# Kernel optimization log

Hardware: AMD Instinct MI355X
Metric: run time of the kernel (lower is better)

Reference implementation:

```python
import jax, jax.numpy as jnp
import numpy as np

NUM_NODES = 100_000
NUM_EDGES = 1_200_000
NUM_REL = 3
EMBED_DIM = 64
HIDDEN_DIM = 64
NUM_CLS = 2
NUM_GRAPHS = 512


def setup_inputs() -> dict:
    key = jax.random.key(0)
    ks = jax.random.split(key, 12)
    s = 1.0 / np.sqrt(EMBED_DIM)
    inp = {
        # forward args
        "x": jnp.zeros((NUM_NODES,), dtype=jnp.int64),  # vocab size 1 -> all zeros
        "edge_index": jax.random.randint(ks[0], (2, NUM_EDGES), 0, NUM_NODES, dtype=jnp.int64),
        "edge_type": jax.random.randint(ks[1], (NUM_EDGES,), 0, NUM_REL, dtype=jnp.int64),
        "batch": jnp.sort(jax.random.randint(ks[2], (NUM_NODES,), 0, NUM_GRAPHS, dtype=jnp.int64)),
        # parameters
        "embed_w": jax.random.normal(ks[3], (1, EMBED_DIM), jnp.float32),
        "W1": jax.random.normal(ks[4], (NUM_REL, EMBED_DIM, HIDDEN_DIM), jnp.float32) * s,
        "root1": jax.random.normal(ks[5], (EMBED_DIM, HIDDEN_DIM), jnp.float32) * s,
        "b1": jnp.zeros((HIDDEN_DIM,), jnp.float32),
        "W2": jax.random.normal(ks[6], (NUM_REL, HIDDEN_DIM, HIDDEN_DIM), jnp.float32) * s,
        "root2": jax.random.normal(ks[7], (HIDDEN_DIM, HIDDEN_DIM), jnp.float32) * s,
        "b2": jnp.zeros((HIDDEN_DIM,), jnp.float32),
        "lin_w": jax.random.normal(ks[8], (HIDDEN_DIM, NUM_CLS), jnp.float32) * s,
        "lin_b": jnp.zeros((NUM_CLS,), jnp.float32),
    }
    return inp


def rgcn_conv(h, W, root, b, src, dst, edge_type):
    """PyG RGCNConv with mean aggregation per relation + root weight + bias."""
    n = h.shape[0]
    out = h @ root + b  # root/self contribution, [N, H]
    for r in range(NUM_REL):
        m = (edge_type == r).astype(h.dtype)  # [E]
        tr = h @ W[r]                          # [N, H] small GEMM
        msg = tr[src] * m[:, None]             # gather [E, H]
        ssum = jax.ops.segment_sum(msg, dst, num_segments=n)  # scatter-add [N, H]
        cnt = jax.ops.segment_sum(m, dst, num_segments=n)     # per-relation in-degree
        out = out + ssum / jnp.clip(cnt, 1.0)[:, None]        # mean aggregation
    return out


def reference(x, edge_index, edge_type, batch, embed_w, W1, root1, b1, W2, root2, b2, lin_w, lin_b):
    src, dst = edge_index[0], edge_index[1]
    h = embed_w[x]                                       # [N, D] embedding lookup
    h = jax.nn.relu(rgcn_conv(h, W1, root1, b1, src, dst, edge_type))
    h = jax.nn.relu(rgcn_conv(h, W2, root2, b2, src, dst, edge_type))
    # global mean pool over graphs
    gsum = jax.ops.segment_sum(h, batch, num_segments=NUM_GRAPHS)            # [G, H]
    gcnt = jax.ops.segment_sum(jnp.ones_like(h[:, 0]), batch, num_segments=NUM_GRAPHS)
    g_emb = gsum / jnp.clip(gcnt, 1.0)[:, None]
    return g_emb @ lin_w + lin_b                          # [G, num_cls]
```

## Files before the change

### kernel.cpp

```cpp
#include <hip/hip_runtime.h>

#define NODES   100000
#define EDGES   1200000
#define NREL    3
#define DIM     64
#define NGRAPH  512

#define BSH     8
#define NB      391
#define BUCKCAP 4096
#define NCH     224
#define CHUNK   5360
#define POISON  0xAAAAAAAAu

#define OFF_PSUM  0
#define OFF_PCNT  4096
#define OFF_DONE  6144
#define OFF_ZEND  6400
#define OFF_CUR   6400
#define OFF_MBN   8448
#define OFF_REC   408832
#define OFF_BASE  6814976
#define OFF_T2    6817024

__global__ __launch_bounds__(512) void k_scat_tab(
        const int* __restrict__ ei, const int* __restrict__ et,
        const float* __restrict__ embed_w, const float* __restrict__ W1,
        const float* __restrict__ root1, const float* __restrict__ b1,
        const float* __restrict__ W2, const float* __restrict__ root2,
        const float* __restrict__ b2,
        unsigned int* __restrict__ cursor, unsigned int* __restrict__ rec,
        unsigned char* __restrict__ mbn,
        float* __restrict__ base, float* __restrict__ T2,
        char* __restrict__ ws) {
    const int tid = threadIdx.x;
    const int bid = blockIdx.x;
    if (bid < 32) {
        {
            uint4* z = (uint4*)ws;
            const int gt = bid * 512 + tid;
            if (gt < OFF_ZEND / 16) z[gt] = make_uint4(0, 0, 0, 0);
        }
        __shared__ float h0[DIM];
        __shared__ float u[DIM];
        __shared__ float t[NREL][DIM];
        __shared__ float h1s[8][DIM];
        __shared__ float red[4][DIM];
        const bool act = tid < 256;
        const int j = tid & 63, w = (tid >> 6) & 3;
        if (act && tid < DIM) h0[tid] = embed_w[tid];
        __syncthreads();
        if (act) {
            const float* M = (w == 0) ? root1 : (W1 + (size_t)(w - 1) * DIM * DIM);
            float s = 0.f;
            for (int k = 0; k < DIM; ++k) s += h0[k] * M[k * DIM + j];
            if (w == 0) u[j] = s + b1[j];
            else        t[w - 1][j] = s;
        }
        __syncthreads();
        if (act) {
            for (int p = w; p < 8; p += 4) {
                float v = u[j];
                if (p & 1) v += t[0][j];
                if (p & 2) v += t[1][j];
                if (p & 4) v += t[2][j];
                h1s[p][j] = fmaxf(v, 0.f);
            }
        }
        __syncthreads();
        const int row = bid;
        const int p = (row < 8) ? row : ((row - 8) & 7);
        if (act) {
            const float* M = (row < 8) ? root2
                                       : (W2 + (size_t)((row - 8) >> 3) * DIM * DIM);
            float s = 0.f;
            for (int k = w * 16; k < w * 16 + 16; ++k) s += h1s[p][k] * M[k * DIM + j];
            red[w][j] = s;
        }
        __syncthreads();
        if (act && w == 0) {
            const float v = red[0][j] + red[1][j] + red[2][j] + red[3][j];
            if (row < 8) base[p * DIM + j] = v + b2[j];
            else         T2[(row - 8) * DIM + j] = v;
        }
        return;
    }
    __shared__ unsigned int   srec[CHUNK];
    __shared__ unsigned short sbkt[CHUNK];
    __shared__ int hist[NB];
    __shared__ int cur[NB];
    for (int b = tid; b < NB; b += 512) hist[b] = 0;
    __syncthreads();
    const int e0 = (bid - 32) * CHUNK;
    const int* src = ei;
    const int* dst = ei + EDGES;
    for (int i = tid; i < CHUNK / 4; i += 512) {
        const int e = e0 + i * 4;
        if (e < EDGES) {
            const int4 s4 = *(const int4*)(src + e);
            const int4 d4 = *(const int4*)(dst + e);
            const int4 r4 = *(const int4*)(et + e);
            const int j = i * 4;
            srec[j + 0] = ((unsigned)(d4.x & 255) << 19) | ((unsigned)r4.x << 17) | (unsigned)s4.x;
            sbkt[j + 0] = (unsigned short)(d4.x >> BSH);
            atomicAdd(&hist[d4.x >> BSH], 1);
            mbn[d4.x * 4 + r4.x] = 1;
            srec[j + 1] = ((unsigned)(d4.y & 255) << 19) | ((unsigned)r4.y << 17) | (unsigned)s4.y;
            sbkt[j + 1] = (unsigned short)(d4.y >> BSH);
            atomicAdd(&hist[d4.y >> BSH], 1);
            mbn[d4.y * 4 + r4.y] = 1;
            srec[j + 2] = ((unsigned)(d4.z & 255) << 19) | ((unsigned)r4.z << 17) | (unsigned)s4.z;
            sbkt[j + 2] = (unsigned short)(d4.z >> BSH);
            atomicAdd(&hist[d4.z >> BSH], 1);
            mbn[d4.z * 4 + r4.z] = 1;
            srec[j + 3] = ((unsigned)(d4.w & 255) << 19) | ((unsigned)r4.w << 17) | (unsigned)s4.w;
            sbkt[j + 3] = (unsigned short)(d4.w >> BSH);
            atomicAdd(&hist[d4.w >> BSH], 1);
            mbn[d4.w * 4 + r4.w] = 1;
        }
    }
    __syncthreads();
    for (int b = tid; b < NB; b += 512) {
        const int h = hist[b];
        unsigned off = 0;
        if (h) off = atomicAdd(&cursor[b], (unsigned)h) - POISON;
        cur[b] = b * BUCKCAP + (int)off;
    }
    __syncthreads();
    int nl = EDGES - e0;
    if (nl > CHUNK) nl = CHUNK;
    for (int i = tid; i < nl; i += 512) {
        const int b = sbkt[i];
        const int p = atomicAdd(&cur[b], 1);
        if (p < (b + 1) * BUCKCAP) rec[p] = srec[i];
    }
}

__global__ __launch_bounds__(1024) void k_node(
        const unsigned int* __restrict__ rec, const unsigned int* __restrict__ cursor,
        const unsigned char* __restrict__ mbn, const int* __restrict__ batch,
        const float* __restrict__ base, const float* __restrict__ T2,
        const float* __restrict__ lin_w, const float* __restrict__ lin_b,
        float* __restrict__ psum, int* __restrict__ pcnt,
        int* __restrict__ done, float* __restrict__ out) {
    __shared__ unsigned int h[3072];
    __shared__ float bs[8 * DIM];
    __shared__ float ts[24 * DIM];
    __shared__ int lastflag;
    const int tid = threadIdx.x;
    const unsigned* mbn32 = (const unsigned*)mbn;
    for (int i = tid; i < 3072; i += 1024) h[i] = 0;
    if (tid < 8 * DIM) bs[tid] = base[tid];
    for (int i = tid; i < 24 * DIM; i += 1024) ts[i] = T2[i];
    __syncthreads();
    const int b = blockIdx.x;
    const int s = b * BUCKCAP;
    unsigned un = cursor[b] - POISON;
    int n = (un > BUCKCAP) ? BUCKCAP : (int)un;
    for (int i = tid; i < n; i += 1024) {
        const unsigned r32 = rec[s + i];
        const unsigned x = mbn32[r32 & 0x1FFFF];
        const int p = (x & 1) | ((x >> 7) & 2) | ((x >> 14) & 4);
        const int idx = (r32 >> 19) * 24 + ((r32 >> 17) & 3) * 8 + p;
        atomicAdd(&h[idx >> 1], 1u << ((idx & 1) * 16));
    }
    __syncthreads();
    const int lane = tid & 63;
    const int w = tid >> 6;
    const int v0 = (b << BSH) + w * 16;
    float dummy = 0.f;
    if (v0 < NODES) {
        const float lw0 = lin_w[lane * 2 + 0];
        const float lw1 = lin_w[lane * 2 + 1];
        int pidx = v0 + (lane & 15);
        if (pidx >= NODES) pidx = NODES - 1;
        const int bv = batch[pidx];
        const int mv = (int)mbn32[pidx];
        float acc = 0.f;
        int curg = -1, runlen = 0;
        for (int i = 0; i < 16; ++i) {
            const int v = v0 + i;
            if (v >= NODES) break;
            const int mx = __shfl(mv, i);
            const int pm = (mx & 1) | ((mx >> 7) & 2) | ((mx >> 14) & 4);
            float sacc = bs[pm * DIM + lane];
            const unsigned* hv = &h[(v & 255) * 12];
            #pragma unroll
            for (int r = 0; r < NREL; ++r) {
                const unsigned x0 = hv[r * 4 + 0], x1 = hv[r * 4 + 1];
                const unsigned x2 = hv[r * 4 + 2], x3 = hv[r * 4 + 3];
                const int cr = (int)((x0 & 0xFFFF) + (x0 >> 16) + (x1 & 0xFFFF) + (x1 >> 16)
                                   + (x2 & 0xFFFF) + (x2 >> 16) + (x3 & 0xFFFF) + (x3 >> 16));
                if (cr > 0) {
                    float msg = 0.f;
                    const float* tr = &ts[r * 8 * DIM + lane];
                    if (x0) msg += (float)(x0 & 0xFFFF) * tr[0 * DIM]
                                 + (float)(x0 >> 16)    * tr[1 * DIM];
                    if (x1) msg += (float)(x1 & 0xFFFF) * tr[2 * DIM]
                                 + (float)(x1 >> 16)    * tr[3 * DIM];
                    if (x2) msg += (float)(x2 & 0xFFFF) * tr[4 * DIM]
                                 + (float)(x2 >> 16)    * tr[5 * DIM];
                    if (x3) msg += (float)(x3 & 0xFFFF) * tr[6 * DIM]
                                 + (float)(x3 >> 16)    * tr[7 * DIM];
                    sacc += msg / (float)cr;
                }
            }
            sacc = fmaxf(sacc, 0.f);
            const int g = __shfl(bv, i);
            if (g != curg) {
                if (curg >= 0) {
                    float p0 = acc * lw0, p1 = acc * lw1;
                    #pragma unroll
                    for (int off = 32; off; off >>= 1) {
                        p0 += __shfl_down(p0, off);
                        p1 += __shfl_down(p1, off);
                    }
                    if (lane == 0) {
                        dummy += atomicAdd(&psum[curg * 2 + 0], p0);
                        dummy += atomicAdd(&psum[curg * 2 + 1], p1);
                        dummy += (float)atomicAdd(&pcnt[curg], runlen);
                    }
                }
                curg = g; acc = 0.f; runlen = 0;
            }
            acc += sacc; runlen++;
        }
        if (curg >= 0) {
            float p0 = acc * lw0, p1 = acc * lw1;
            #pragma unroll
            for (int off = 32; off; off >>= 1) {
                p0 += __shfl_down(p0, off);
                p1 += __shfl_down(p1, off);
            }
            if (lane == 0) {
                dummy += atomicAdd(&psum[curg * 2 + 0], p0);
                dummy += atomicAdd(&psum[curg * 2 + 1], p1);
                dummy += (float)atomicAdd(&pcnt[curg], runlen);
            }
        }
    }
    asm volatile("" :: "v"(dummy));
    __syncthreads();
    if (tid == 0) lastflag = (atomicAdd(done, 1) == NB - 1) ? 1 : 0;
    __syncthreads();
    if (lastflag && tid < NGRAPH) {
        const float q0 = atomicAdd(&psum[tid * 2 + 0], 0.0f);
        const float q1 = atomicAdd(&psum[tid * 2 + 1], 0.0f);
        const int   c  = atomicAdd(&pcnt[tid], 0);
        const float inv = 1.0f / fmaxf((float)c, 1.0f);
        out[tid * 2 + 0] = q0 * inv + lin_b[0];
        out[tid * 2 + 1] = q1 * inv + lin_b[1];
    }
}

extern "C" void kernel_launch(void* const* d_in, const int* in_sizes, int n_in,
                              void* d_out, int out_size, void* d_ws, size_t ws_size,
                              hipStream_t stream) {
    const int*   ei      = (const int*)d_in[1];
    const int*   et      = (const int*)d_in[2];
    const int*   batch   = (const int*)d_in[3];
    const float* embed_w = (const float*)d_in[4];
    const float* W1      = (const float*)d_in[5];
    const float* root1   = (const float*)d_in[6];
    const float* b1      = (const float*)d_in[7];
    const float* W2      = (const float*)d_in[8];
    const float* root2   = (const float*)d_in[9];
    const float* b2      = (const float*)d_in[10];
    const float* lin_w   = (const float*)d_in[11];
    const float* lin_b   = (const float*)d_in[12];
    float* out = (float*)d_out;

    char* ws = (char*)d_ws;
    float*         psum = (float*)(ws + OFF_PSUM);
    int*           pcnt = (int*)(ws + OFF_PCNT);
    int*           done = (int*)(ws + OFF_DONE);
    unsigned int*  cur  = (unsigned int*)(ws + OFF_CUR);
    unsigned char* mbn  = (unsigned char*)(ws + OFF_MBN);
    unsigned int*  rec  = (unsigned int*)(ws + OFF_REC);
    float*         base = (float*)(ws + OFF_BASE);
    float*         T2   = (float*)(ws + OFF_T2);

    k_scat_tab<<<256, 512,  0, stream>>>(ei, et, embed_w, W1, root1, b1, W2, root2,
                                         b2, cur, rec, mbn, base, T2, (char*)d_ws);
    k_node    <<<NB,  1024, 0, stream>>>(rec, cur, mbn, batch, base, T2, lin_w,
                                         lin_b, psum, pcnt, done, out);
}
```

Baseline: 139.4 us.

## Split node buckets into quarter-blocks and unroll scatter loads for memory parallelism

k_node now runs four 512-thread blocks per 256-node bucket. Each block filters the bucket's records by destination quarter and keeps a smaller shared histogram, and each wave prefetches the next node's counters into registers. In k_scat_tab the edge-load and scatter loops are manually unrolled so several int4 loads and atomics are in flight per thread. The aim is more blocks and more memory-level parallelism, at the cost of every record being read four times (once per quarter block) and more atomics on the completion counter.

New measurement: 152.8 us. +9.6%, slower.

```diff
diff --git a/kernel.cpp b/kernel.cpp
--- a/kernel.cpp
+++ b/kernel.cpp
@@ -8,6 +8,7 @@
 
 #define BSH     8
 #define NB      391
+#define NBK2    1564
 #define BUCKCAP 4096
 #define NCH     224
 #define CHUNK   5360
@@ -94,29 +95,60 @@
     const int e0 = (bid - 32) * CHUNK;
     const int* src = ei;
     const int* dst = ei + EDGES;
-    for (int i = tid; i < CHUNK / 4; i += 512) {
-        const int e = e0 + i * 4;
-        if (e < EDGES) {
-            const int4 s4 = *(const int4*)(src + e);
-            const int4 d4 = *(const int4*)(dst + e);
-            const int4 r4 = *(const int4*)(et + e);
-            const int j = i * 4;
-            srec[j + 0] = ((unsigned)(d4.x & 255) << 19) | ((unsigned)r4.x << 17) | (unsigned)s4.x;
-            sbkt[j + 0] = (unsigned short)(d4.x >> BSH);
-            atomicAdd(&hist[d4.x >> BSH], 1);
-            mbn[d4.x * 4 + r4.x] = 1;
-            srec[j + 1] = ((unsigned)(d4.y & 255) << 19) | ((unsigned)r4.y << 17) | (unsigned)s4.y;
-            sbkt[j + 1] = (unsigned short)(d4.y >> BSH);
-            atomicAdd(&hist[d4.y >> BSH], 1);
-            mbn[d4.y * 4 + r4.y] = 1;
-            srec[j + 2] = ((unsigned)(d4.z & 255) << 19) | ((unsigned)r4.z << 17) | (unsigned)s4.z;
-            sbkt[j + 2] = (unsigned short)(d4.z >> BSH);
-            atomicAdd(&hist[d4.z >> BSH], 1);
-            mbn[d4.z * 4 + r4.z] = 1;
-            srec[j + 3] = ((unsigned)(d4.w & 255) << 19) | ((unsigned)r4.w << 17) | (unsigned)s4.w;
-            sbkt[j + 3] = (unsigned short)(d4.w >> BSH);
-            atomicAdd(&hist[d4.w >> BSH], 1);
-            mbn[d4.w * 4 + r4.w] = 1;
+    {
+        const int g0 = tid, g1 = tid + 512, g2 = tid + 1024;
+        const int ea = e0 + g0 * 4, eb = e0 + g1 * 4, ec = e0 + g2 * 4;
+        const bool a0 = (g0 < CHUNK / 4) && (ea < EDGES);
+        const bool a1 = (g1 < CHUNK / 4) && (eb < EDGES);
+        const bool a2 = (g2 < CHUNK / 4) && (ec < EDGES);
+        int4 sa, da, ra, sb, db, rb, sc, dc, rc;
+        if (a0) { sa = *(const int4*)(src + ea); da = *(const int4*)(dst + ea); ra = *(const int4*)(et + ea); }
+        if (a1) { sb = *(const int4*)(src + eb); db = *(const int4*)(dst + eb); rb = *(const int4*)(et + eb); }
+        if (a2) { sc = *(const int4*)(src + ec); dc = *(const int4*)(dst + ec); rc = *(const int4*)(et + ec); }
+        if (a0) {
+            const int j = g0 * 4;
+            srec[j + 0] = ((unsigned)(da.x & 255) << 19) | ((unsigned)ra.x << 17) | (unsigned)sa.x;
+            srec[j + 1] = ((unsigned)(da.y & 255) << 19) | ((unsigned)ra.y << 17) | (unsigned)sa.y;
+            srec[j + 2] = ((unsigned)(da.z & 255) << 19) | ((unsigned)ra.z << 17) | (unsigned)sa.z;
+            srec[j + 3] = ((unsigned)(da.w & 255) << 19) | ((unsigned)ra.w << 17) | (unsigned)sa.w;
+            sbkt[j + 0] = (unsigned short)(da.x >> BSH);
+            sbkt[j + 1] = (unsigned short)(da.y >> BSH);
+            sbkt[j + 2] = (unsigned short)(da.z >> BSH);
+            sbkt[j + 3] = (unsigned short)(da.w >> BSH);
+            atomicAdd(&hist[da.x >> BSH], 1); atomicAdd(&hist[da.y >> BSH], 1);
+            atomicAdd(&hist[da.z >> BSH], 1); atomicAdd(&hist[da.w >> BSH], 1);
+            mbn[da.x * 4 + ra.x] = 1; mbn[da.y * 4 + ra.y] = 1;
+            mbn[da.z * 4 + ra.z] = 1; mbn[da.w * 4 + ra.w] = 1;
+        }
+        if (a1) {
+            const int j = g1 * 4;
+            srec[j + 0] = ((unsigned)(db.x & 255) << 19) | ((unsigned)rb.x << 17) | (unsigned)sb.x;
+            srec[j + 1] = ((unsigned)(db.y & 255) << 19) | ((unsigned)rb.y << 17) | (unsigned)sb.y;
+            srec[j + 2] = ((unsigned)(db.z & 255) << 19) | ((unsigned)rb.z << 17) | (unsigned)sb.z;
+            srec[j + 3] = ((unsigned)(db.w & 255) << 19) | ((unsigned)rb.w << 17) | (unsigned)sb.w;
+            sbkt[j + 0] = (unsigned short)(db.x >> BSH);
+            sbkt[j + 1] = (unsigned short)(db.y >> BSH);
+            sbkt[j + 2] = (unsigned short)(db.z >> BSH);
+            sbkt[j + 3] = (unsigned short)(db.w >> BSH);
+            atomicAdd(&hist[db.x >> BSH], 1); atomicAdd(&hist[db.y >> BSH], 1);
+            atomicAdd(&hist[db.z >> BSH], 1); atomicAdd(&hist[db.w >> BSH], 1);
+            mbn[db.x * 4 + rb.x] = 1; mbn[db.y * 4 + rb.y] = 1;
+            mbn[db.z * 4 + rb.z] = 1; mbn[db.w * 4 + rb.w] = 1;
+        }
+        if (a2) {
+            const int j = g2 * 4;
+            srec[j + 0] = ((unsigned)(dc.x & 255) << 19) | ((unsigned)rc.x << 17) | (unsigned)sc.x;
+            srec[j + 1] = ((unsigned)(dc.y & 255) << 19) | ((unsigned)rc.y << 17) | (unsigned)sc.y;
+            srec[j + 2] = ((unsigned)(dc.z & 255) << 19) | ((unsigned)rc.z << 17) | (unsigned)sc.z;
+            srec[j + 3] = ((unsigned)(dc.w & 255) << 19) | ((unsigned)rc.w << 17) | (unsigned)sc.w;
+            sbkt[j + 0] = (unsigned short)(dc.x >> BSH);
+            sbkt[j + 1] = (unsigned short)(dc.y >> BSH);
+            sbkt[j + 2] = (unsigned short)(dc.z >> BSH);
+            sbkt[j + 3] = (unsigned short)(dc.w >> BSH);
+            atomicAdd(&hist[dc.x >> BSH], 1); atomicAdd(&hist[dc.y >> BSH], 1);
+            atomicAdd(&hist[dc.z >> BSH], 1); atomicAdd(&hist[dc.w >> BSH], 1);
+            mbn[dc.x * 4 + rc.x] = 1; mbn[dc.y * 4 + rc.y] = 1;
+            mbn[dc.z * 4 + rc.z] = 1; mbn[dc.w * 4 + rc.w] = 1;
         }
     }
     __syncthreads();
@@ -129,79 +161,150 @@
     __syncthreads();
     int nl = EDGES - e0;
     if (nl > CHUNK) nl = CHUNK;
-    for (int i = tid; i < nl; i += 512) {
-        const int b = sbkt[i];
-        const int p = atomicAdd(&cur[b], 1);
-        if (p < (b + 1) * BUCKCAP) rec[p] = srec[i];
+    for (int j = 0; j < 11; j += 2) {
+        const int i0 = tid + j * 512, i1 = tid + (j + 1) * 512;
+        const bool a0 = i0 < nl, a1 = i1 < nl;
+        int b0 = 0, b1 = 0; unsigned v0 = 0, v1 = 0;
+        if (a0) { b0 = sbkt[i0]; v0 = srec[i0]; }
+        if (a1) { b1 = sbkt[i1]; v1 = srec[i1]; }
+        int p0 = 0, p1 = 0;
+        if (a0) p0 = atomicAdd(&cur[b0], 1);
+        if (a1) p1 = atomicAdd(&cur[b1], 1);
+        if (a0 && p0 < (b0 + 1) * BUCKCAP) rec[p0] = v0;
+        if (a1 && p1 < (b1 + 1) * BUCKCAP) rec[p1] = v1;
     }
 }
 
-__global__ __launch_bounds__(1024) void k_node(
+__global__ __launch_bounds__(512) void k_node(
         const unsigned int* __restrict__ rec, const unsigned int* __restrict__ cursor,
         const unsigned char* __restrict__ mbn, const int* __restrict__ batch,
         const float* __restrict__ base, const float* __restrict__ T2,
         const float* __restrict__ lin_w, const float* __restrict__ lin_b,
         float* __restrict__ psum, int* __restrict__ pcnt,
         int* __restrict__ done, float* __restrict__ out) {
-    __shared__ unsigned int h[3072];
+    __shared__ unsigned int h[768];
     __shared__ float bs[8 * DIM];
     __shared__ float ts[24 * DIM];
     __shared__ int lastflag;
     const int tid = threadIdx.x;
     const unsigned* mbn32 = (const unsigned*)mbn;
-    for (int i = tid; i < 3072; i += 1024) h[i] = 0;
-    if (tid < 8 * DIM) bs[tid] = base[tid];
-    for (int i = tid; i < 24 * DIM; i += 1024) ts[i] = T2[i];
-    __syncthreads();
-    const int b = blockIdx.x;
+    if (tid < 256) { h[tid] = 0; h[tid + 256] = 0; h[tid + 512] = 0; }
+    bs[tid] = base[tid];
+    ts[tid] = T2[tid]; ts[tid + 512] = T2[tid + 512]; ts[tid + 1024] = T2[tid + 1024];
+    __syncthreads();
+    const int bid = blockIdx.x;
+    const int b = bid >> 2, q = bid & 3;
     const int s = b * BUCKCAP;
-    unsigned un = cursor[b] - POISON;
-    int n = (un > BUCKCAP) ? BUCKCAP : (int)un;
-    for (int i = tid; i < n; i += 1024) {
-        const unsigned r32 = rec[s + i];
-        const unsigned x = mbn32[r32 & 0x1FFFF];
-        const int p = (x & 1) | ((x >> 7) & 2) | ((x >> 14) & 4);
-        const int idx = (r32 >> 19) * 24 + ((r32 >> 17) & 3) * 8 + p;
-        atomicAdd(&h[idx >> 1], 1u << ((idx & 1) * 16));
+    const unsigned un = cursor[b] - POISON;
+    const int n = (un > BUCKCAP) ? BUCKCAP : (int)un;
+    #pragma unroll
+    for (int hf = 0; hf < 2; ++hf) {
+        const int i0 = tid + hf * 2048, i1 = i0 + 512, i2 = i0 + 1024, i3 = i0 + 1536;
+        unsigned r0 = 0, r1 = 0, r2 = 0, r3 = 0;
+        const bool a0 = i0 < n, a1 = i1 < n, a2 = i2 < n, a3 = i3 < n;
+        if (a0) r0 = rec[s + i0];
+        if (a1) r1 = rec[s + i1];
+        if (a2) r2 = rec[s + i2];
+        if (a3) r3 = rec[s + i3];
+        const bool q0 = a0 && (int)((r0 >> 25) & 3) == q;
+        const bool q1 = a1 && (int)((r1 >> 25) & 3) == q;
+        const bool q2 = a2 && (int)((r2 >> 25) & 3) == q;
+        const bool q3 = a3 && (int)((r3 >> 25) & 3) == q;
+        unsigned x0 = 0, x1 = 0, x2 = 0, x3 = 0;
+        if (q0) x0 = mbn32[r0 & 0x1FFFF];
+        if (q1) x1 = mbn32[r1 & 0x1FFFF];
+        if (q2) x2 = mbn32[r2 & 0x1FFFF];
+        if (q3) x3 = mbn32[r3 & 0x1FFFF];
+        if (q0) {
+            const int p = (x0 & 1) | ((x0 >> 7) & 2) | ((x0 >> 14) & 4);
+            const int idx = (int)((r0 >> 19) & 63) * 24 + (int)((r0 >> 17) & 3) * 8 + p;
+            atomicAdd(&h[idx >> 1], 1u << ((idx & 1) * 16));
+        }
+        if (q1) {
+            const int p = (x1 & 1) | ((x1 >> 7) & 2) | ((x1 >> 14) & 4);
+            const int idx = (int)((r1 >> 19) & 63) * 24 + (int)((r1 >> 17) & 3) * 8 + p;
+            atomicAdd(&h[idx >> 1], 1u << ((idx & 1) * 16));
+        }
+        if (q2) {
+            const int p = (x2 & 1) | ((x2 >> 7) & 2) | ((x2 >> 14) & 4);
+            const int idx = (int)((r2 >> 19) & 63) * 24 + (int)((r2 >> 17) & 3) * 8 + p;
+            atomicAdd(&h[idx >> 1], 1u << ((idx & 1) * 16));
+        }
+        if (q3) {
+            const int p = (x3 & 1) | ((x3 >> 7) & 2) | ((x3 >> 14) & 4);
+            const int idx = (int)((r3 >> 19) & 63) * 24 + (int)((r3 >> 17) & 3) * 8 + p;
+            atomicAdd(&h[idx >> 1], 1u << ((idx & 1) * 16));
+        }
     }
     __syncthreads();
     const int lane = tid & 63;
     const int w = tid >> 6;
-    const int v0 = (b << BSH) + w * 16;
+    const int v0 = (b << 8) + q * 64 + w * 8;
     float dummy = 0.f;
     if (v0 < NODES) {
         const float lw0 = lin_w[lane * 2 + 0];
         const float lw1 = lin_w[lane * 2 + 1];
-        int pidx = v0 + (lane & 15);
+        int pidx = v0 + (lane & 7);
         if (pidx >= NODES) pidx = NODES - 1;
         const int bv = batch[pidx];
         const int mv = (int)mbn32[pidx];
+        const unsigned* hb = &h[(w * 8) * 12];
+        unsigned c0 = hb[0], c1 = hb[1], c2 = hb[2],  c3 = hb[3];
+        unsigned c4 = hb[4], c5 = hb[5], c6 = hb[6],  c7 = hb[7];
+        unsigned c8 = hb[8], c9 = hb[9], c10 = hb[10], c11 = hb[11];
         float acc = 0.f;
         int curg = -1, runlen = 0;
-        for (int i = 0; i < 16; ++i) {
+        for (int i = 0; i < 8; ++i) {
             const int v = v0 + i;
             if (v >= NODES) break;
+            unsigned e0 = 0, e1 = 0, e2 = 0, e3 = 0, e4 = 0, e5 = 0;
+            unsigned e6 = 0, e7 = 0, e8 = 0, e9 = 0, e10 = 0, e11 = 0;
+            const bool nx = (i + 1 < 8) && (v + 1 < NODES);
+            if (nx) {
+                const unsigned* nb = &h[(w * 8 + i + 1) * 12];
+                e0 = nb[0]; e1 = nb[1]; e2 = nb[2];  e3 = nb[3];
+                e4 = nb[4]; e5 = nb[5]; e6 = nb[6];  e7 = nb[7];
+                e8 = nb[8]; e9 = nb[9]; e10 = nb[10]; e11 = nb[11];
+            }
             const int mx = __shfl(mv, i);
             const int pm = (mx & 1) | ((mx >> 7) & 2) | ((mx >> 14) & 4);
             float sacc = bs[pm * DIM + lane];
-            const unsigned* hv = &h[(v & 255) * 12];
-            #pragma unroll
-            for (int r = 0; r < NREL; ++r) {
-                const unsigned x0 = hv[r * 4 + 0], x1 = hv[r * 4 + 1];
-                const unsigned x2 = hv[r * 4 + 2], x3 = hv[r * 4 + 3];
-                const int cr = (int)((x0 & 0xFFFF) + (x0 >> 16) + (x1 & 0xFFFF) + (x1 >> 16)
-                                   + (x2 & 0xFFFF) + (x2 >> 16) + (x3 & 0xFFFF) + (x3 >> 16));
+            {
+                const int cr = (int)((c0 & 0xFFFF) + (c0 >> 16) + (c1 & 0xFFFF) + (c1 >> 16)
+                                   + (c2 & 0xFFFF) + (c2 >> 16) + (c3 & 0xFFFF) + (c3 >> 16));
                 if (cr > 0) {
                     float msg = 0.f;
-                    const float* tr = &ts[r * 8 * DIM + lane];
-                    if (x0) msg += (float)(x0 & 0xFFFF) * tr[0 * DIM]
-                                 + (float)(x0 >> 16)    * tr[1 * DIM];
-                    if (x1) msg += (float)(x1 & 0xFFFF) * tr[2 * DIM]
-                                 + (float)(x1 >> 16)    * tr[3 * DIM];
-                    if (x2) msg += (float)(x2 & 0xFFFF) * tr[4 * DIM]
-                                 + (float)(x2 >> 16)    * tr[5 * DIM];
-                    if (x3) msg += (float)(x3 & 0xFFFF) * tr[6 * DIM]
-                                 + (float)(x3 >> 16)    * tr[7 * DIM];
+                    const float* tr = &ts[lane];
+                    if (c0) msg += (float)(c0 & 0xFFFF) * tr[0 * DIM] + (float)(c0 >> 16) * tr[1 * DIM];
+                    if (c1) msg += (float)(c1 & 0xFFFF) * tr[2 * DIM] + (float)(c1 >> 16) * tr[3 * DIM];
+                    if (c2) msg += (float)(c2 & 0xFFFF) * tr[4 * DIM] + (float)(c2 >> 16) * tr[5 * DIM];
+                    if (c3) msg += (float)(c3 & 0xFFFF) * tr[6 * DIM] + (float)(c3 >> 16) * tr[7 * DIM];
+                    sacc += msg / (float)cr;
+                }
+            }
+            {
+                const int cr = (int)((c4 & 0xFFFF) + (c4 >> 16) + (c5 & 0xFFFF) + (c5 >> 16)
+                                   + (c6 & 0xFFFF) + (c6 >> 16) + (c7 & 0xFFFF) + (c7 >> 16));
+                if (cr > 0) {
+                    float msg = 0.f;
+                    const float* tr = &ts[8 * DIM + lane];
+                    if (c4) msg += (float)(c4 & 0xFFFF) * tr[0 * DIM] + (float)(c4 >> 16) * tr[1 * DIM];
+                    if (c5) msg += (float)(c5 & 0xFFFF) * tr[2 * DIM] + (float)(c5 >> 16) * tr[3 * DIM];
+                    if (c6) msg += (float)(c6 & 0xFFFF) * tr[4 * DIM] + (float)(c6 >> 16) * tr[5 * DIM];
+                    if (c7) msg += (float)(c7 & 0xFFFF) * tr[6 * DIM] + (float)(c7 >> 16) * tr[7 * DIM];
+                    sacc += msg / (float)cr;
+                }
+            }
+            {
+                const int cr = (int)((c8 & 0xFFFF) + (c8 >> 16) + (c9 & 0xFFFF) + (c9 >> 16)
+                                   + (c10 & 0xFFFF) + (c10 >> 16) + (c11 & 0xFFFF) + (c11 >> 16));
+                if (cr > 0) {
+                    float msg = 0.f;
+                    const float* tr = &ts[16 * DIM + lane];
+                    if (c8)  msg += (float)(c8 & 0xFFFF)  * tr[0 * DIM] + (float)(c8 >> 16)  * tr[1 * DIM];
+                    if (c9)  msg += (float)(c9 & 0xFFFF)  * tr[2 * DIM] + (float)(c9 >> 16)  * tr[3 * DIM];
+                    if (c10) msg += (float)(c10 & 0xFFFF) * tr[4 * DIM] + (float)(c10 >> 16) * tr[5 * DIM];
+                    if (c11) msg += (float)(c11 & 0xFFFF) * tr[6 * DIM] + (float)(c11 >> 16) * tr[7 * DIM];
                     sacc += msg / (float)cr;
                 }
             }
@@ -224,6 +327,9 @@
                 curg = g; acc = 0.f; runlen = 0;
             }
             acc += sacc; runlen++;
+            c0 = e0; c1 = e1; c2 = e2;  c3 = e3;
+            c4 = e4; c5 = e5; c6 = e6;  c7 = e7;
+            c8 = e8; c9 = e9; c10 = e10; c11 = e11;
         }
         if (curg >= 0) {
             float p0 = acc * lw0, p1 = acc * lw1;
@@ -241,7 +347,7 @@
     }
     asm volatile("" :: "v"(dummy));
     __syncthreads();
-    if (tid == 0) lastflag = (atomicAdd(done, 1) == NB - 1) ? 1 : 0;
+    if (tid == 0) lastflag = (atomicAdd(done, 1) == NBK2 - 1) ? 1 : 0;
     __syncthreads();
     if (lastflag && tid < NGRAPH) {
         const float q0 = atomicAdd(&psum[tid * 2 + 0], 0.0f);
@@ -280,8 +386,8 @@
     float*         base = (float*)(ws + OFF_BASE);
     float*         T2   = (float*)(ws + OFF_T2);
 
-    k_scat_tab<<<256, 512,  0, stream>>>(ei, et, embed_w, W1, root1, b1, W2, root2,
+    k_scat_tab<<<256,  512, 0, stream>>>(ei, et, embed_w, W1, root1, b1, W2, root2,
                                          b2, cur, rec, mbn, base, T2, (char*)d_ws);
-    k_node    <<<NB,  1024, 0, stream>>>(rec, cur, mbn, batch, base, T2, lin_w,
+    k_node    <<<NBK2, 512, 0, stream>>>(rec, cur, mbn, batch, base, T2, lin_w,
                                          lin_b, psum, pcnt, done, out);
 }
```
